# Kernel tuning notes

Measured on AMD Instinct MI355X. Metric: run time of the kernel, lower is better.

Reference implementation:

```python
import jax, jax.numpy as jnp
from jax import lax
import numpy as np

V, H, L, C, T = 32000, 1024, 256, 32, 64
SOS_TOKEN = 0


def _lstm_cell(h, c, x, Wih, Whh, bih, bhh):
    # h,c,x: [1,H]; Wih,Whh: [4H,H] (torch gate order i,f,g,o)
    g = x @ Wih.T + h @ Whh.T + bih + bhh
    i, f, gg, o = jnp.split(g, 4, axis=-1)
    c = jax.nn.sigmoid(f) * c + jax.nn.sigmoid(i) * jnp.tanh(gg)
    h = jax.nn.sigmoid(o) * jnp.tanh(c)
    return h, c


def setup_inputs() -> dict:
    key = jax.random.key(0)
    ks = jax.random.split(key, 24)
    s = 1.0 / np.sqrt(H)
    n = lambda k, shp, sc: (jax.random.normal(k, shp, dtype=jnp.float32) * sc)
    return {
        "word": jax.random.randint(ks[0], (1, T), 0, V),
        "tense": jax.random.randint(ks[1], (1,), 0, 4),
        "use_teacher_forcing": 1,
        "tense_emb": n(ks[2], (4, C), 0.02),
        "enc_emb": n(ks[3], (V, H), 0.02),
        "enc_Wih": n(ks[4], (4 * H, H), s),
        "enc_Whh": n(ks[5], (4 * H, H), s),
        "enc_bih": n(ks[6], (4 * H,), s),
        "enc_bhh": n(ks[7], (4 * H,), s),
        "W_mean": n(ks[8], (L, H), s),
        "b_mean": n(ks[9], (L,), s),
        "W_var": n(ks[10], (L, H), s),
        "b_var": n(ks[11], (L,), s),
        "W_l2h": n(ks[12], (H, L + C), s),
        "b_l2h": n(ks[13], (H,), s),
        "dec_emb": n(ks[14], (V, H), 0.02),
        "dec_Wih": n(ks[15], (4 * H, H), s),
        "dec_Whh": n(ks[16], (4 * H, H), s),
        "dec_bih": n(ks[17], (4 * H,), s),
        "dec_bhh": n(ks[18], (4 * H,), s),
        "W_out": n(ks[19], (V, H), s),
        "b_out": n(ks[20], (V,), s),
        "eps": jax.random.normal(ks[21], (L,), dtype=jnp.float32),
    }


def reference(word, tense, use_teacher_forcing, tense_emb, enc_emb, enc_Wih,
              enc_Whh, enc_bih, enc_bhh, W_mean, b_mean, W_var, b_var,
              W_l2h, b_l2h, dec_emb, dec_Wih, dec_Whh, dec_bih, dec_bhh,
              W_out, b_out, eps):
    tense_e = tense_emb[tense]                       # [1, C]
    # Encoder: initial hidden = [zeros(H-C) | tense_emb]
    h0 = jnp.concatenate([jnp.zeros((1, H - C), tense_e.dtype), tense_e], axis=-1)
    c0 = jnp.zeros((1, H), tense_e.dtype)
    enc_x = enc_emb[word[0]]                         # [T, H]

    def enc_step(carry, x):
        h, c = _lstm_cell(carry[0], carry[1], x[None], enc_Wih, enc_Whh, enc_bih, enc_bhh)
        return (h, c), None

    (h, _c), _ = lax.scan(enc_step, (h0, c0), enc_x)
    mean = h @ W_mean.T + b_mean                     # [1, L]
    logvar = h @ W_var.T + b_var                     # [1, L]
    latent = mean + eps * jnp.exp(0.5 * logvar)      # reparameterize

    dec_h0 = jnp.concatenate([latent, tense_e], axis=-1) @ W_l2h.T + b_l2h  # [1,H]
    dec_c0 = jnp.zeros((1, H), dec_h0.dtype)

    # teacher forcing: inputs are [SOS, word[0][0], ..., word[0][T-2]]
    dec_in = jnp.concatenate([jnp.full((1,), SOS_TOKEN, word.dtype), word[0, :-1]])
    dec_x = jax.nn.relu(dec_emb[dec_in])             # [T, H]

    def dec_step(carry, x):
        h, c = _lstm_cell(carry[0], carry[1], x[None], dec_Wih, dec_Whh, dec_bih, dec_bhh)
        logits = h @ W_out.T + b_out                 # [1, V]
        return (h, c), jax.nn.log_softmax(logits, axis=-1)[0]

    _, pred_distribution = lax.scan(dec_step, (dec_h0, dec_c0), dec_x)  # [T, V]
    pred_output = jnp.argmax(pred_distribution, axis=1)                 # [T]
    return pred_output, pred_distribution, mean, logvar
```

## Files before the change

kernel.cpp:

```cpp
#include <hip/hip_runtime.h>
#include <math.h>

#define Hd 1024
#define Td 64
#define Vd 32000

static const size_t OFF_ENCX  = 0;
static const size_t OFF_DECX  = 65536;
static const size_t OFF_GENC  = 131072;
static const size_t OFF_GDEC  = 393216;
static const size_t OFF_BSE   = 655360;
static const size_t OFF_BSD   = 659456;
static const size_t OFF_TEN   = 663552;
static const size_t OFF_HALL  = 663584;
static const size_t OFF_STATS = 729120;
static const size_t OFF_MB    = 730144;

#define MB_H_PAIRS  133120u
#define MB_PAIRS    133376u
#define FLAGB       0x3f800000u

__device__ __forceinline__ float fsigm(float x) {
  return __fdividef(1.f, 1.f + __expf(-x));
}
__device__ __forceinline__ float ftanh(float x) {
  return 1.f - __fdividef(2.f, __expf(2.f * x) + 1.f);
}

__device__ __forceinline__ void st_flag(unsigned long long* p, float v) {
  unsigned long long u = 0x3f80000000000000ull | (unsigned long long)__float_as_uint(v);
  __hip_atomic_store(p, u, __ATOMIC_RELAXED, __HIP_MEMORY_SCOPE_AGENT);
}

__device__ __forceinline__ float4 poll16(const float2* p) {
  float4 a;
  for (;;) {
    asm volatile("global_load_dwordx4 %0, %1, off sc0 sc1\n\ts_waitcnt vmcnt(0)"
                 : "=&v"(a) : "v"(p) : "memory");
    if (__float_as_uint(a.y) == FLAGB && __float_as_uint(a.w) == FLAGB) return a;
  }
}

__device__ __forceinline__ void stage1024(const float2* base, float* dst, int tid) {
  float4 a = poll16(base + 2 * tid);
  ((float2*)dst)[tid] = make_float2(a.x, a.z);
  __syncthreads();
}

__global__ void prep_kernel(const int* __restrict__ word, const int* __restrict__ tense,
                            const float* __restrict__ tense_emb,
                            const float* __restrict__ enc_emb, const float* __restrict__ dec_emb,
                            const float* __restrict__ enc_bih, const float* __restrict__ enc_bhh,
                            const float* __restrict__ dec_bih, const float* __restrict__ dec_bhh,
                            float* __restrict__ ws) {
  int gid = blockIdx.x * blockDim.x + threadIdx.x;
  int gsz = gridDim.x * blockDim.x;
  int tens = tense[0];
  for (int i = gid; i < Td * Hd; i += gsz) {
    int t = i >> 10, hh = i & 1023;
    ws[OFF_ENCX + i] = enc_emb[(size_t)word[t] * Hd + hh];
    int tok = (t == 0) ? 0 : word[t - 1];
    float v = dec_emb[(size_t)tok * Hd + hh];
    ws[OFF_DECX + i] = v > 0.f ? v : 0.f;
  }
  for (int i = gid; i < 4096; i += gsz) {
    ws[OFF_BSE + i] = enc_bih[i] + enc_bhh[i];
    ws[OFF_BSD + i] = dec_bih[i] + dec_bhh[i];
  }
  for (int i = gid; i < 32; i += gsz) ws[OFF_TEN + i] = tense_emb[tens * 32 + i];
  float2* mb = (float2*)(ws + OFF_MB);
  for (int i = gid; i < (int)MB_PAIRS; i += gsz) {
    float2 v;
    if (i < (int)MB_H_PAIRS && (i >> 10) == 0) {
      int j = i & 1023;
      v.x = (j < Hd - 32) ? 0.f : tense_emb[tens * 32 + (j - (Hd - 32))];
      v.y = 1.0f;
    } else { v.x = 0.f; v.y = 0.f; }
    mb[i] = v;
  }
}

__device__ __forceinline__ void gemm_body(const float* __restrict__ W,
                                          const float* __restrict__ x,
                                          const float* __restrict__ bias,
                                          float* __restrict__ out, int R, int rbase) {
  __shared__ float xs[64][68];
  __shared__ float wsh[64][68];
  const int tid = threadIdx.x;
  const int a = tid >> 4;
  const int b = tid & 15;
  const int sr = tid & 63;
  const int kq = (tid >> 6) << 4;
  float acc[4][4];
#pragma unroll
  for (int i = 0; i < 4; ++i)
#pragma unroll
    for (int q = 0; q < 4; ++q) acc[i][q] = 0.f;

  for (int kc = 0; kc < 1024; kc += 64) {
    const float4* gx = (const float4*)(x + (size_t)sr * 1024 + kc + kq);
    const float4* gw = (const float4*)(W + (size_t)(rbase + sr) * 1024 + kc + kq);
    float4 vx0 = gx[0], vx1 = gx[1], vx2 = gx[2], vx3 = gx[3];
    float4 vw0 = gw[0], vw1 = gw[1], vw2 = gw[2], vw3 = gw[3];
    __syncthreads();
    xs[kq +  0][sr] = vx0.x; xs[kq +  1][sr] = vx0.y; xs[kq +  2][sr] = vx0.z; xs[kq +  3][sr] = vx0.w;
    xs[kq +  4][sr] = vx1.x; xs[kq +  5][sr] = vx1.y; xs[kq +  6][sr] = vx1.z; xs[kq +  7][sr] = vx1.w;
    xs[kq +  8][sr] = vx2.x; xs[kq +  9][sr] = vx2.y; xs[kq + 10][sr] = vx2.z; xs[kq + 11][sr] = vx2.w;
    xs[kq + 12][sr] = vx3.x; xs[kq + 13][sr] = vx3.y; xs[kq + 14][sr] = vx3.z; xs[kq + 15][sr] = vx3.w;
    wsh[kq +  0][sr] = vw0.x; wsh[kq +  1][sr] = vw0.y; wsh[kq +  2][sr] = vw0.z; wsh[kq +  3][sr] = vw0.w;
    wsh[kq +  4][sr] = vw1.x; wsh[kq +  5][sr] = vw1.y; wsh[kq +  6][sr] = vw1.z; wsh[kq +  7][sr] = vw1.w;
    wsh[kq +  8][sr] = vw2.x; wsh[kq +  9][sr] = vw2.y; wsh[kq + 10][sr] = vw2.z; wsh[kq + 11][sr] = vw2.w;
    wsh[kq + 12][sr] = vw3.x; wsh[kq + 13][sr] = vw3.y; wsh[kq + 14][sr] = vw3.z; wsh[kq + 15][sr] = vw3.w;
    __syncthreads();
#pragma unroll 8
    for (int kk = 0; kk < 64; ++kk) {
      float4 xv = *(const float4*)&xs[kk][a * 4];
      float4 wv = *(const float4*)&wsh[kk][b * 4];
      acc[0][0] = fmaf(xv.x, wv.x, acc[0][0]); acc[0][1] = fmaf(xv.x, wv.y, acc[0][1]);
      acc[0][2] = fmaf(xv.x, wv.z, acc[0][2]); acc[0][3] = fmaf(xv.x, wv.w, acc[0][3]);
      acc[1][0] = fmaf(xv.y, wv.x, acc[1][0]); acc[1][1] = fmaf(xv.y, wv.y, acc[1][1]);
      acc[1][2] = fmaf(xv.y, wv.z, acc[1][2]); acc[1][3] = fmaf(xv.y, wv.w, acc[1][3]);
      acc[2][0] = fmaf(xv.z, wv.x, acc[2][0]); acc[2][1] = fmaf(xv.z, wv.y, acc[2][1]);
      acc[2][2] = fmaf(xv.z, wv.z, acc[2][2]); acc[2][3] = fmaf(xv.z, wv.w, acc[2][3]);
      acc[3][0] = fmaf(xv.w, wv.x, acc[3][0]); acc[3][1] = fmaf(xv.w, wv.y, acc[3][1]);
      acc[3][2] = fmaf(xv.w, wv.z, acc[3][2]); acc[3][3] = fmaf(xv.w, wv.w, acc[3][3]);
    }
  }
  const int rb = rbase + b * 4;
  float4 bv = *(const float4*)(bias + rb);
#pragma unroll
  for (int i = 0; i < 4; ++i) {
    int t = a * 4 + i;
    float4 o;
    o.x = acc[i][0] + bv.x; o.y = acc[i][1] + bv.y;
    o.z = acc[i][2] + bv.z; o.w = acc[i][3] + bv.w;
    *(float4*)(out + (size_t)t * R + rb) = o;
  }
}

__global__ __launch_bounds__(256, 2) void gemm_kernel(const float* __restrict__ W,
                                                      const float* __restrict__ x,
                                                      const float* __restrict__ bias,
                                                      float* __restrict__ out, int R) {
  gemm_body(W, x, bias, out, R, blockIdx.x * 64);
}

__global__ __launch_bounds__(256, 2) void gemm_dual_kernel(
    const float* __restrict__ W0, const float* __restrict__ x0,
    const float* __restrict__ b0, float* __restrict__ o0,
    const float* __restrict__ W1, const float* __restrict__ x1,
    const float* __restrict__ b1, float* __restrict__ o1) {
  if (blockIdx.x < 64) gemm_body(W0, x0, b0, o0, 4096, blockIdx.x * 64);
  else                 gemm_body(W1, x1, b1, o1, 4096, (blockIdx.x - 64) * 64);
}

__device__ __forceinline__ void gload16(const float* base, float* d) {
  asm volatile(
      "global_load_dword %0, %16, off\n\t"
      "global_load_dword %1, %16, off offset:256\n\t"
      "global_load_dword %2, %16, off offset:512\n\t"
      "global_load_dword %3, %16, off offset:768\n\t"
      "global_load_dword %4, %16, off offset:1024\n\t"
      "global_load_dword %5, %16, off offset:1280\n\t"
      "global_load_dword %6, %16, off offset:1536\n\t"
      "global_load_dword %7, %16, off offset:1792\n\t"
      "global_load_dword %8, %16, off offset:2048\n\t"
      "global_load_dword %9, %16, off offset:2304\n\t"
      "global_load_dword %10, %16, off offset:2560\n\t"
      "global_load_dword %11, %16, off offset:2816\n\t"
      "global_load_dword %12, %16, off offset:3072\n\t"
      "global_load_dword %13, %16, off offset:3328\n\t"
      "global_load_dword %14, %16, off offset:3584\n\t"
      "global_load_dword %15, %16, off offset:3840\n\t"
      "s_waitcnt vmcnt(0)"
      : "=&v"(d[0]), "=&v"(d[1]), "=&v"(d[2]), "=&v"(d[3]),
        "=&v"(d[4]), "=&v"(d[5]), "=&v"(d[6]), "=&v"(d[7]),
        "=&v"(d[8]), "=&v"(d[9]), "=&v"(d[10]), "=&v"(d[11]),
        "=&v"(d[12]), "=&v"(d[13]), "=&v"(d[14]), "=&v"(d[15])
      : "v"(base));
}

__global__ __launch_bounds__(512, 2) void seq_kernel(
    const float* __restrict__ enc_Whh, const float* __restrict__ dec_Whh,
    const float* __restrict__ W_mean, const float* __restrict__ b_mean,
    const float* __restrict__ W_var, const float* __restrict__ b_var,
    const float* __restrict__ W_l2h, const float* __restrict__ b_l2h,
    const float* __restrict__ eps, float* __restrict__ ws, float* __restrict__ dout) {
  __shared__ float hsbuf[2][Hd];
  __shared__ float lat[288];
  const int tid = threadIdx.x;
  const int lane = tid & 63;
  const int wid = tid >> 6;
  const int j = blockIdx.x * 8 + wid;

  float2* mb = (float2*)(ws + OFF_MB);
  unsigned long long* mbq = (unsigned long long*)(ws + OFF_MB);
  const float* Genc = ws + OFF_GENC;
  const float* Gdec = ws + OFF_GDEC;
  float* h_all = ws + OFF_HALL;

  float we[4][16], wd[4][16];
#pragma unroll
  for (int r = 0; r < 4; ++r) {
    const size_t ro = (size_t)(r * Hd + j) * Hd + lane;
    gload16(enc_Whh + ro, we[r]);
    gload16(dec_Whh + ro, wd[r]);
  }

  float c_reg = 0.f;
  float gb0 = Genc[j], gb1 = Genc[1024 + j], gb2 = Genc[2048 + j], gb3 = Genc[3072 + j];
  for (int t = 0; t < Td; ++t) {
    stage1024(mb + (size_t)t * 1024, hsbuf[t & 1], tid);
    const float* hs = hsbuf[t & 1];
    float p0 = 0.f, p1 = 0.f, p2 = 0.f, p3 = 0.f;
#pragma unroll
    for (int i = 0; i < 16; ++i) {
      float hv = hs[lane + 64 * i];
      p0 = fmaf(we[0][i], hv, p0);
      p1 = fmaf(we[1][i], hv, p1);
      p2 = fmaf(we[2][i], hv, p2);
      p3 = fmaf(we[3][i], hv, p3);
    }
#pragma unroll
    for (int off = 32; off; off >>= 1) {
      p0 += __shfl_xor(p0, off, 64); p1 += __shfl_xor(p1, off, 64);
      p2 += __shfl_xor(p2, off, 64); p3 += __shfl_xor(p3, off, 64);
    }
    float gi = gb0 + p0, gf = gb1 + p1, gg = gb2 + p2, go = gb3 + p3;
    c_reg = fsigm(gf) * c_reg + fsigm(gi) * ftanh(gg);
    float hval = fsigm(go) * ftanh(c_reg);
    if (lane == 0) st_flag(mbq + (size_t)(t + 1) * 1024 + j, hval);
    if (t + 1 < Td) {
      gb0 = Genc[(t + 1) * 4096 + j];
      gb1 = Genc[(t + 1) * 4096 + 1024 + j];
      gb2 = Genc[(t + 1) * 4096 + 2048 + j];
      gb3 = Genc[(t + 1) * 4096 + 3072 + j];
    }
  }

  if (j < 256) {
    stage1024(mb + (size_t)Td * 1024, hsbuf[0], tid);
    const float* hs = hsbuf[0];
    const float* Wm = W_mean + (size_t)j * Hd;
    const float* Wv = W_var + (size_t)j * Hd;
    float pm = 0.f, pv = 0.f;
#pragma unroll
    for (int i = 0; i < 16; ++i) {
      float hv = hs[lane + 64 * i];
      pm = fmaf(Wm[lane + 64 * i], hv, pm);
      pv = fmaf(Wv[lane + 64 * i], hv, pv);
    }
#pragma unroll
    for (int off = 32; off; off >>= 1) {
      pm += __shfl_xor(pm, off, 64); pv += __shfl_xor(pv, off, 64);
    }
    if (lane == 0) {
      float m = pm + b_mean[j];
      float lv = pv + b_var[j];
      dout[2048064 + j] = m;
      dout[2048320 + j] = lv;
      float latv = m + eps[j] * __expf(0.5f * lv);
      st_flag(mbq + MB_H_PAIRS + j, latv);
    }
  }

  if (tid < 128) {
    float4 a = poll16(mb + MB_H_PAIRS + 2 * tid);
    lat[2 * tid] = a.x; lat[2 * tid + 1] = a.z;
  } else if (tid < 160) {
    lat[256 + (tid - 128)] = ws[OFF_TEN + (tid - 128)];
  }
  __syncthreads();

  {
    const float* Wr = W_l2h + (size_t)j * 288;
    float p = fmaf(Wr[lane], lat[lane], 0.f);
    p = fmaf(Wr[lane + 64], lat[lane + 64], p);
    p = fmaf(Wr[lane + 128], lat[lane + 128], p);
    p = fmaf(Wr[lane + 192], lat[lane + 192], p);
    if (lane < 32) p = fmaf(Wr[lane + 256], lat[lane + 256], p);
#pragma unroll
    for (int off = 32; off; off >>= 1) p += __shfl_xor(p, off, 64);
    if (lane == 0) st_flag(mbq + (size_t)65 * 1024 + j, p + b_l2h[j]);
  }
  __syncthreads();

  c_reg = 0.f;
  gb0 = Gdec[j]; gb1 = Gdec[1024 + j]; gb2 = Gdec[2048 + j]; gb3 = Gdec[3072 + j];
  for (int t = 0; t < Td; ++t) {
    stage1024(mb + (size_t)(65 + t) * 1024, hsbuf[t & 1], tid);
    const float* hs = hsbuf[t & 1];
    float p0 = 0.f, p1 = 0.f, p2 = 0.f, p3 = 0.f;
#pragma unroll
    for (int i = 0; i < 16; ++i) {
      float hv = hs[lane + 64 * i];
      p0 = fmaf(wd[0][i], hv, p0);
      p1 = fmaf(wd[1][i], hv, p1);
      p2 = fmaf(wd[2][i], hv, p2);
      p3 = fmaf(wd[3][i], hv, p3);
    }
#pragma unroll
    for (int off = 32; off; off >>= 1) {
      p0 += __shfl_xor(p0, off, 64); p1 += __shfl_xor(p1, off, 64);
      p2 += __shfl_xor(p2, off, 64); p3 += __shfl_xor(p3, off, 64);
    }
    float gi = gb0 + p0, gf = gb1 + p1, gg = gb2 + p2, go = gb3 + p3;
    c_reg = fsigm(gf) * c_reg + fsigm(gi) * ftanh(gg);
    float hval = fsigm(go) * ftanh(c_reg);
    if (lane == 0) {
      if (t + 1 < Td) st_flag(mbq + (size_t)(66 + t) * 1024 + j, hval);
      h_all[(size_t)t * Hd + j] = hval;
    }
    if (t + 1 < Td) {
      gb0 = Gdec[(t + 1) * 4096 + j];
      gb1 = Gdec[(t + 1) * 4096 + 1024 + j];
      gb2 = Gdec[(t + 1) * 4096 + 2048 + j];
      gb3 = Gdec[(t + 1) * 4096 + 3072 + j];
    }
  }
}

__global__ __launch_bounds__(256) void lstats_kernel(const float* __restrict__ logits,
                                                     float* __restrict__ sd) {
  const int blk = blockIdx.x, t = blk >> 2, q = blk & 3, tid = threadIdx.x;
  const float* row = logits + (size_t)t * Vd + q * 8000;
  __shared__ float sm[256];
  __shared__ int si[256];
  float m = -INFINITY; int mi = 0x7fffffff;
  for (int v = tid; v < 8000; v += 256) {
    float x = row[v];
    if (x > m) { m = x; mi = v; }
  }
  sm[tid] = m; si[tid] = mi;
  __syncthreads();
  for (int s = 128; s > 0; s >>= 1) {
    if (tid < s) {
      float om = sm[tid + s]; int oi = si[tid + s];
      if (om > sm[tid] || (om == sm[tid] && oi < si[tid])) { sm[tid] = om; si[tid] = oi; }
    }
    __syncthreads();
  }
  float rm = sm[0]; int ri = si[0];
  __syncthreads();
  float s = 0.f;
  for (int v = tid; v < 8000; v += 256) s += __expf(row[v] - rm);
  sm[tid] = s;
  __syncthreads();
  for (int st = 128; st > 0; st >>= 1) {
    if (tid < st) sm[tid] += sm[tid + st];
    __syncthreads();
  }
  if (tid == 0) {
    sd[blk * 4 + 0] = rm;
    sd[blk * 4 + 1] = (float)(ri + q * 8000);
    sd[blk * 4 + 2] = sm[0];
  }
}

__global__ __launch_bounds__(256) void lfin_kernel(float* __restrict__ out,
                                                   const float* __restrict__ sd) {
  const int blk = blockIdx.x, t = blk >> 2, q = blk & 3, tid = threadIdx.x;
  float M = -INFINITY;
#pragma unroll
  for (int k = 0; k < 4; ++k) M = fmaxf(M, sd[t * 16 + k * 4]);
  float S = 0.f;
#pragma unroll
  for (int k = 0; k < 4; ++k) S += sd[t * 16 + k * 4 + 2] * __expf(sd[t * 16 + k * 4] - M);
  float corr = M + logf(S);
  float4* r4 = (float4*)(out + 64 + (size_t)t * Vd + q * 8000);
  for (int i = tid; i < 2000; i += 256) {
    float4 v = r4[i];
    v.x -= corr; v.y -= corr; v.z -= corr; v.w -= corr;
    r4[i] = v;
  }
  if (q == 0 && tid == 0) {
    float bm = -INFINITY; int bi = 0;
#pragma unroll
    for (int k = 0; k < 4; ++k) {
      float m = sd[t * 16 + k * 4];
      if (m > bm) { bm = m; bi = (int)sd[t * 16 + k * 4 + 1]; }
    }
    out[t] = (float)bi;
  }
}

extern "C" void kernel_launch(void* const* d_in, const int* in_sizes, int n_in,
                              void* d_out, int out_size, void* d_ws, size_t ws_size,
                              hipStream_t stream) {
  (void)in_sizes; (void)n_in; (void)out_size; (void)ws_size;
  const int* word       = (const int*)d_in[0];
  const int* tense      = (const int*)d_in[1];
  const float* tense_emb = (const float*)d_in[3];
  const float* enc_emb   = (const float*)d_in[4];
  const float* enc_Wih   = (const float*)d_in[5];
  const float* enc_Whh   = (const float*)d_in[6];
  const float* enc_bih   = (const float*)d_in[7];
  const float* enc_bhh   = (const float*)d_in[8];
  const float* W_mean    = (const float*)d_in[9];
  const float* b_mean    = (const float*)d_in[10];
  const float* W_var     = (const float*)d_in[11];
  const float* b_var     = (const float*)d_in[12];
  const float* W_l2h     = (const float*)d_in[13];
  const float* b_l2h     = (const float*)d_in[14];
  const float* dec_emb   = (const float*)d_in[15];
  const float* dec_Wih   = (const float*)d_in[16];
  const float* dec_Whh   = (const float*)d_in[17];
  const float* dec_bih   = (const float*)d_in[18];
  const float* dec_bhh   = (const float*)d_in[19];
  const float* W_out     = (const float*)d_in[20];
  const float* b_out     = (const float*)d_in[21];
  const float* eps       = (const float*)d_in[22];
  float* out = (float*)d_out;
  float* ws  = (float*)d_ws;

  prep_kernel<<<512, 256, 0, stream>>>(word, tense, tense_emb, enc_emb, dec_emb,
                                       enc_bih, enc_bhh, dec_bih, dec_bhh, ws);
  gemm_dual_kernel<<<128, 256, 0, stream>>>(enc_Wih, ws + OFF_ENCX, ws + OFF_BSE, ws + OFF_GENC,
                                            dec_Wih, ws + OFF_DECX, ws + OFF_BSD, ws + OFF_GDEC);
  seq_kernel<<<128, 512, 0, stream>>>(enc_Whh, dec_Whh, W_mean, b_mean, W_var, b_var,
                                      W_l2h, b_l2h, eps, ws, out);
  gemm_kernel<<<500, 256, 0, stream>>>(W_out, ws + OFF_HALL, b_out, out + 64, 32000);
  lstats_kernel<<<256, 256, 0, stream>>>(out + 64, ws + OFF_STATS);
  lfin_kernel<<<256, 256, 0, stream>>>(out, ws + OFF_STATS);
}
```

Baseline: 519.0 us.

## Widen GEMM tiles to 128 rows and fuse log-softmax into one LDS-resident kernel

The shared GEMM body now computes a 64x128 tile per block with 4x8 outputs per thread instead of 64x64. This halves the block count for the input-projection and output-projection GEMMs and improves arithmetic intensity per LDS load, at the cost of more registers and fewer blocks to fill the CUs. Separately, the two-kernel split log-softmax/argmax is replaced by one kernel per timestep that stages the 32000-wide row in LDS. That removes a launch and a global re-read but leaves only 64 blocks of work.

```diff
diff --git a/kernel.cpp b/kernel.cpp
--- a/kernel.cpp
+++ b/kernel.cpp
@@ -13,7 +13,6 @@
 static const size_t OFF_BSD   = 659456;
 static const size_t OFF_TEN   = 663552;
 static const size_t OFF_HALL  = 663584;
-static const size_t OFF_STATS = 729120;
 static const size_t OFF_MB    = 730144;
 
 #define MB_H_PAIRS  133120u
@@ -85,56 +84,81 @@
                                           const float* __restrict__ bias,
                                           float* __restrict__ out, int R, int rbase) {
   __shared__ float xs[64][68];
-  __shared__ float wsh[64][68];
+  __shared__ float wsh[64][132];
   const int tid = threadIdx.x;
   const int a = tid >> 4;
   const int b = tid & 15;
-  const int sr = tid & 63;
-  const int kq = (tid >> 6) << 4;
-  float acc[4][4];
+  const int sxr = tid & 63;
+  const int sxk = (tid >> 6) << 4;
+  const int swr = tid & 127;
+  const int swk = (tid >> 7) << 5;
+  float acc[4][8];
 #pragma unroll
   for (int i = 0; i < 4; ++i)
 #pragma unroll
-    for (int q = 0; q < 4; ++q) acc[i][q] = 0.f;
+    for (int q = 0; q < 8; ++q) acc[i][q] = 0.f;
 
   for (int kc = 0; kc < 1024; kc += 64) {
-    const float4* gx = (const float4*)(x + (size_t)sr * 1024 + kc + kq);
-    const float4* gw = (const float4*)(W + (size_t)(rbase + sr) * 1024 + kc + kq);
-    float4 vx0 = gx[0], vx1 = gx[1], vx2 = gx[2], vx3 = gx[3];
-    float4 vw0 = gw[0], vw1 = gw[1], vw2 = gw[2], vw3 = gw[3];
+    float4 vx[4];
+    const float4* gx = (const float4*)(x + (size_t)sxr * 1024 + kc + sxk);
+#pragma unroll
+    for (int m = 0; m < 4; ++m) vx[m] = gx[m];
+    float4 vw[8];
+    const float4* gw = (const float4*)(W + (size_t)(rbase + swr) * 1024 + kc + swk);
+#pragma unroll
+    for (int m = 0; m < 8; ++m) vw[m] = gw[m];
     __syncthreads();
-    xs[kq +  0][sr] = vx0.x; xs[kq +  1][sr] = vx0.y; xs[kq +  2][sr] = vx0.z; xs[kq +  3][sr] = vx0.w;
-    xs[kq +  4][sr] = vx1.x; xs[kq +  5][sr] = vx1.y; xs[kq +  6][sr] = vx1.z; xs[kq +  7][sr] = vx1.w;
-    xs[kq +  8][sr] = vx2.x; xs[kq +  9][sr] = vx2.y; xs[kq + 10][sr] = vx2.z; xs[kq + 11][sr] = vx2.w;
-    xs[kq + 12][sr] = vx3.x; xs[kq + 13][sr] = vx3.y; xs[kq + 14][sr] = vx3.z; xs[kq + 15][sr] = vx3.w;
-    wsh[kq +  0][sr] = vw0.x; wsh[kq +  1][sr] = vw0.y; wsh[kq +  2][sr] = vw0.z; wsh[kq +  3][sr] = vw0.w;
-    wsh[kq +  4][sr] = vw1.x; wsh[kq +  5][sr] = vw1.y; wsh[kq +  6][sr] = vw1.z; wsh[kq +  7][sr] = vw1.w;
-    wsh[kq +  8][sr] = vw2.x; wsh[kq +  9][sr] = vw2.y; wsh[kq + 10][sr] = vw2.z; wsh[kq + 11][sr] = vw2.w;
-    wsh[kq + 12][sr] = vw3.x; wsh[kq + 13][sr] = vw3.y; wsh[kq + 14][sr] = vw3.z; wsh[kq + 15][sr] = vw3.w;
+#pragma unroll
+    for (int m = 0; m < 4; ++m) {
+      xs[sxk + 4 * m + 0][sxr] = vx[m].x;
+      xs[sxk + 4 * m + 1][sxr] = vx[m].y;
+      xs[sxk + 4 * m + 2][sxr] = vx[m].z;
+      xs[sxk + 4 * m + 3][sxr] = vx[m].w;
+    }
+#pragma unroll
+    for (int m = 0; m < 8; ++m) {
+      wsh[swk + 4 * m + 0][swr] = vw[m].x;
+      wsh[swk + 4 * m + 1][swr] = vw[m].y;
+      wsh[swk + 4 * m + 2][swr] = vw[m].z;
+      wsh[swk + 4 * m + 3][swr] = vw[m].w;
+    }
     __syncthreads();
-#pragma unroll 8
+#pragma unroll 4
     for (int kk = 0; kk < 64; ++kk) {
-      float4 xv = *(const float4*)&xs[kk][a * 4];
-      float4 wv = *(const float4*)&wsh[kk][b * 4];
-      acc[0][0] = fmaf(xv.x, wv.x, acc[0][0]); acc[0][1] = fmaf(xv.x, wv.y, acc[0][1]);
-      acc[0][2] = fmaf(xv.x, wv.z, acc[0][2]); acc[0][3] = fmaf(xv.x, wv.w, acc[0][3]);
-      acc[1][0] = fmaf(xv.y, wv.x, acc[1][0]); acc[1][1] = fmaf(xv.y, wv.y, acc[1][1]);
-      acc[1][2] = fmaf(xv.y, wv.z, acc[1][2]); acc[1][3] = fmaf(xv.y, wv.w, acc[1][3]);
-      acc[2][0] = fmaf(xv.z, wv.x, acc[2][0]); acc[2][1] = fmaf(xv.z, wv.y, acc[2][1]);
-      acc[2][2] = fmaf(xv.z, wv.z, acc[2][2]); acc[2][3] = fmaf(xv.z, wv.w, acc[2][3]);
-      acc[3][0] = fmaf(xv.w, wv.x, acc[3][0]); acc[3][1] = fmaf(xv.w, wv.y, acc[3][1]);
-      acc[3][2] = fmaf(xv.w, wv.z, acc[3][2]); acc[3][3] = fmaf(xv.w, wv.w, acc[3][3]);
-    }
-  }
-  const int rb = rbase + b * 4;
-  float4 bv = *(const float4*)(bias + rb);
+      float4 xv  = *(const float4*)&xs[kk][a * 4];
+      float4 wv0 = *(const float4*)&wsh[kk][b * 8];
+      float4 wv1 = *(const float4*)&wsh[kk][b * 8 + 4];
+      acc[0][0]=fmaf(xv.x,wv0.x,acc[0][0]); acc[0][1]=fmaf(xv.x,wv0.y,acc[0][1]);
+      acc[0][2]=fmaf(xv.x,wv0.z,acc[0][2]); acc[0][3]=fmaf(xv.x,wv0.w,acc[0][3]);
+      acc[0][4]=fmaf(xv.x,wv1.x,acc[0][4]); acc[0][5]=fmaf(xv.x,wv1.y,acc[0][5]);
+      acc[0][6]=fmaf(xv.x,wv1.z,acc[0][6]); acc[0][7]=fmaf(xv.x,wv1.w,acc[0][7]);
+      acc[1][0]=fmaf(xv.y,wv0.x,acc[1][0]); acc[1][1]=fmaf(xv.y,wv0.y,acc[1][1]);
+      acc[1][2]=fmaf(xv.y,wv0.z,acc[1][2]); acc[1][3]=fmaf(xv.y,wv0.w,acc[1][3]);
+      acc[1][4]=fmaf(xv.y,wv1.x,acc[1][4]); acc[1][5]=fmaf(xv.y,wv1.y,acc[1][5]);
+      acc[1][6]=fmaf(xv.y,wv1.z,acc[1][6]); acc[1][7]=fmaf(xv.y,wv1.w,acc[1][7]);
+      acc[2][0]=fmaf(xv.z,wv0.x,acc[2][0]); acc[2][1]=fmaf(xv.z,wv0.y,acc[2][1]);
+      acc[2][2]=fmaf(xv.z,wv0.z,acc[2][2]); acc[2][3]=fmaf(xv.z,wv0.w,acc[2][3]);
+      acc[2][4]=fmaf(xv.z,wv1.x,acc[2][4]); acc[2][5]=fmaf(xv.z,wv1.y,acc[2][5]);
+      acc[2][6]=fmaf(xv.z,wv1.z,acc[2][6]); acc[2][7]=fmaf(xv.z,wv1.w,acc[2][7]);
+      acc[3][0]=fmaf(xv.w,wv0.x,acc[3][0]); acc[3][1]=fmaf(xv.w,wv0.y,acc[3][1]);
+      acc[3][2]=fmaf(xv.w,wv0.z,acc[3][2]); acc[3][3]=fmaf(xv.w,wv0.w,acc[3][3]);
+      acc[3][4]=fmaf(xv.w,wv1.x,acc[3][4]); acc[3][5]=fmaf(xv.w,wv1.y,acc[3][5]);
+      acc[3][6]=fmaf(xv.w,wv1.z,acc[3][6]); acc[3][7]=fmaf(xv.w,wv1.w,acc[3][7]);
+    }
+  }
+  const int rb = rbase + b * 8;
+  float4 bv0 = *(const float4*)(bias + rb);
+  float4 bv1 = *(const float4*)(bias + rb + 4);
 #pragma unroll
   for (int i = 0; i < 4; ++i) {
     int t = a * 4 + i;
-    float4 o;
-    o.x = acc[i][0] + bv.x; o.y = acc[i][1] + bv.y;
-    o.z = acc[i][2] + bv.z; o.w = acc[i][3] + bv.w;
-    *(float4*)(out + (size_t)t * R + rb) = o;
+    float4 o0, o1;
+    o0.x = acc[i][0] + bv0.x; o0.y = acc[i][1] + bv0.y;
+    o0.z = acc[i][2] + bv0.z; o0.w = acc[i][3] + bv0.w;
+    o1.x = acc[i][4] + bv1.x; o1.y = acc[i][5] + bv1.y;
+    o1.z = acc[i][6] + bv1.z; o1.w = acc[i][7] + bv1.w;
+    *(float4*)(out + (size_t)t * R + rb) = o0;
+    *(float4*)(out + (size_t)t * R + rb + 4) = o1;
   }
 }
 
@@ -142,7 +166,7 @@
                                                       const float* __restrict__ x,
                                                       const float* __restrict__ bias,
                                                       float* __restrict__ out, int R) {
-  gemm_body(W, x, bias, out, R, blockIdx.x * 64);
+  gemm_body(W, x, bias, out, R, blockIdx.x * 128);
 }
 
 __global__ __launch_bounds__(256, 2) void gemm_dual_kernel(
@@ -150,8 +174,8 @@
     const float* __restrict__ b0, float* __restrict__ o0,
     const float* __restrict__ W1, const float* __restrict__ x1,
     const float* __restrict__ b1, float* __restrict__ o1) {
-  if (blockIdx.x < 64) gemm_body(W0, x0, b0, o0, 4096, blockIdx.x * 64);
-  else                 gemm_body(W1, x1, b1, o1, 4096, (blockIdx.x - 64) * 64);
+  if (blockIdx.x < 32) gemm_body(W0, x0, b0, o0, 4096, blockIdx.x * 128);
+  else                 gemm_body(W1, x1, b1, o1, 4096, (blockIdx.x - 32) * 128);
 }
 
 __device__ __forceinline__ void gload16(const float* base, float* d) {
@@ -320,20 +344,24 @@
   }
 }
 
-__global__ __launch_bounds__(256) void lstats_kernel(const float* __restrict__ logits,
-                                                     float* __restrict__ sd) {
-  const int blk = blockIdx.x, t = blk >> 2, q = blk & 3, tid = threadIdx.x;
-  const float* row = logits + (size_t)t * Vd + q * 8000;
-  __shared__ float sm[256];
-  __shared__ int si[256];
-  float m = -INFINITY; int mi = 0x7fffffff;
-  for (int v = tid; v < 8000; v += 256) {
+__global__ __launch_bounds__(512, 1) void logsm_kernel(float* __restrict__ out) {
+  __shared__ float row[Vd];
+  __shared__ float sm[512];
+  __shared__ int si[512];
+  const int t = blockIdx.x, tid = threadIdx.x;
+  float* gr = out + 64 + (size_t)t * Vd;
+  float4* gr4 = (float4*)gr;
+  float4* r4 = (float4*)row;
+  for (int i = tid; i < Vd / 4; i += 512) r4[i] = gr4[i];
+  __syncthreads();
+  float m = -INFINITY; int mi = 0;
+  for (int v = tid; v < Vd; v += 512) {
     float x = row[v];
     if (x > m) { m = x; mi = v; }
   }
   sm[tid] = m; si[tid] = mi;
   __syncthreads();
-  for (int s = 128; s > 0; s >>= 1) {
+  for (int s = 256; s > 0; s >>= 1) {
     if (tid < s) {
       float om = sm[tid + s]; int oi = si[tid + s];
       if (om > sm[tid] || (om == sm[tid] && oi < si[tid])) { sm[tid] = om; si[tid] = oi; }
@@ -343,45 +371,20 @@
   float rm = sm[0]; int ri = si[0];
   __syncthreads();
   float s = 0.f;
-  for (int v = tid; v < 8000; v += 256) s += __expf(row[v] - rm);
+  for (int v = tid; v < Vd; v += 512) s += __expf(row[v] - rm);
   sm[tid] = s;
   __syncthreads();
-  for (int st = 128; st > 0; st >>= 1) {
+  for (int st = 256; st > 0; st >>= 1) {
     if (tid < st) sm[tid] += sm[tid + st];
     __syncthreads();
   }
-  if (tid == 0) {
-    sd[blk * 4 + 0] = rm;
-    sd[blk * 4 + 1] = (float)(ri + q * 8000);
-    sd[blk * 4 + 2] = sm[0];
-  }
-}
-
-__global__ __launch_bounds__(256) void lfin_kernel(float* __restrict__ out,
-                                                   const float* __restrict__ sd) {
-  const int blk = blockIdx.x, t = blk >> 2, q = blk & 3, tid = threadIdx.x;
-  float M = -INFINITY;
-#pragma unroll
-  for (int k = 0; k < 4; ++k) M = fmaxf(M, sd[t * 16 + k * 4]);
-  float S = 0.f;
-#pragma unroll
-  for (int k = 0; k < 4; ++k) S += sd[t * 16 + k * 4 + 2] * __expf(sd[t * 16 + k * 4] - M);
-  float corr = M + logf(S);
-  float4* r4 = (float4*)(out + 64 + (size_t)t * Vd + q * 8000);
-  for (int i = tid; i < 2000; i += 256) {
+  float corr = rm + logf(sm[0]);
+  for (int i = tid; i < Vd / 4; i += 512) {
     float4 v = r4[i];
     v.x -= corr; v.y -= corr; v.z -= corr; v.w -= corr;
-    r4[i] = v;
-  }
-  if (q == 0 && tid == 0) {
-    float bm = -INFINITY; int bi = 0;
-#pragma unroll
-    for (int k = 0; k < 4; ++k) {
-      float m = sd[t * 16 + k * 4];
-      if (m > bm) { bm = m; bi = (int)sd[t * 16 + k * 4 + 1]; }
-    }
-    out[t] = (float)bi;
-  }
+    gr4[i] = v;
+  }
+  if (tid == 0) out[t] = (float)ri;
 }
 
 extern "C" void kernel_launch(void* const* d_in, const int* in_sizes, int n_in,
@@ -415,11 +418,10 @@
 
   prep_kernel<<<512, 256, 0, stream>>>(word, tense, tense_emb, enc_emb, dec_emb,
                                        enc_bih, enc_bhh, dec_bih, dec_bhh, ws);
-  gemm_dual_kernel<<<128, 256, 0, stream>>>(enc_Wih, ws + OFF_ENCX, ws + OFF_BSE, ws + OFF_GENC,
-                                            dec_Wih, ws + OFF_DECX, ws + OFF_BSD, ws + OFF_GDEC);
+  gemm_dual_kernel<<<64, 256, 0, stream>>>(enc_Wih, ws + OFF_ENCX, ws + OFF_BSE, ws + OFF_GENC,
+                                           dec_Wih, ws + OFF_DECX, ws + OFF_BSD, ws + OFF_GDEC);
   seq_kernel<<<128, 512, 0, stream>>>(enc_Whh, dec_Whh, W_mean, b_mean, W_var, b_var,
                                       W_l2h, b_l2h, eps, ws, out);
-  gemm_kernel<<<500, 256, 0, stream>>>(W_out, ws + OFF_HALL, b_out, out + 64, 32000);
-  lstats_kernel<<<256, 256, 0, stream>>>(out + 64, ws + OFF_STATS);
-  lfin_kernel<<<256, 256, 0, stream>>>(out, ws + OFF_STATS);
-}
+  gemm_kernel<<<250, 256, 0, stream>>>(W_out, ws + OFF_HALL, b_out, out + 64, 32000);
+  logsm_kernel<<<64, 512, 0, stream>>>(out);
+}
```

New measurement: 571.0 us. 10.0% more time.
